# Optimization experiments

Measured on AMD Instinct MI355X. Metric: run time of the kernel, lower is better.

## Reference

```python
import jax, jax.numpy as jnp
import numpy as np

N, E, D, R = 50000, 600000, 128, 8


def rgcn_conv(x, src, dst, etype, W, root, bias):
    """PyG-style RGCNConv with mean aggregation per relation.
    x: [N, Din]; W: [R, Din, Dout]; root: [Din, Dout]; bias: [Dout]."""
    n = x.shape[0]
    r = W.shape[0]
    # Transform once per relation at node level (cheaper than per-edge matmul).
    xw = jnp.einsum('nd,rdo->rno', x, W)  # [R, N, Dout]
    # Per-(relation, target) edge counts for mean normalization.
    seg = etype * n + dst                  # combined segment id in [0, R*N)
    counts = jax.ops.segment_sum(jnp.ones(src.shape, dtype=x.dtype), seg,
                                 num_segments=r * n)
    norm = 1.0 / jnp.maximum(counts[seg], 1.0)   # [E]
    msg = xw[etype, src] * norm[:, None]          # gather per edge, [E, Dout]
    agg = jax.ops.segment_sum(msg, dst, num_segments=n)  # scatter-add, [N, Dout]
    return agg + x @ root + bias


def setup_inputs() -> dict:
    key = jax.random.key(0)
    ks = jax.random.split(key, 16)
    s = 1.0 / np.sqrt(D)
    inp = {
        'x': jax.random.normal(ks[0], (N, D), dtype=jnp.float32),
        'edge_index': jax.random.randint(ks[1], (2, E), 0, N, dtype=jnp.int32),
        'edge_type': jax.random.randint(ks[2], (E,), 0, R, dtype=jnp.int32),
        'W1': jax.random.normal(ks[3], (R, D, D), dtype=jnp.float32) * s,
        'root1': jax.random.normal(ks[4], (D, D), dtype=jnp.float32) * s,
        'b1': jnp.zeros((D,), dtype=jnp.float32),
        'W2': jax.random.normal(ks[5], (R, D, D), dtype=jnp.float32) * s,
        'root2': jax.random.normal(ks[6], (D, D), dtype=jnp.float32) * s,
        'b2': jnp.zeros((D,), dtype=jnp.float32),
        'W3': jax.random.normal(ks[7], (R, D, D), dtype=jnp.float32) * s,
        'root3': jax.random.normal(ks[8], (D, D), dtype=jnp.float32) * s,
        'b3': jnp.zeros((D,), dtype=jnp.float32),
        'res_w': jax.random.normal(ks[9], (D, D), dtype=jnp.float32) * s,
        'res_b': jnp.zeros((D,), dtype=jnp.float32),
    }
    return inp


def reference(x, edge_index, edge_type, W1, root1, b1, W2, root2, b2,
              W3, root3, b3, res_w, res_b):
    src, dst = edge_index[0], edge_index[1]
    res = x @ res_w + res_b
    h = jax.nn.relu(rgcn_conv(x, src, dst, edge_type, W1, root1, b1))
    h = res + jax.nn.relu(h)
    h = jax.nn.relu(rgcn_conv(h, src, dst, edge_type, W2, root2, b2))
    h = res + jax.nn.relu(h)
    h = jax.nn.relu(rgcn_conv(h, src, dst, edge_type, W3, root3, b3))
    h = res + jax.nn.relu(h)
    # Dropout(0.05) is identity in eval mode.
    return h
```

## Files before the change

### kernel.cpp

```cpp
#include <hip/hip_runtime.h>
#include <hip/hip_bf16.h>

#define NN 50000
#define EE 600000
#define RR 8
#define NSEG (NN*RR)
#define NB_SCAN ((NSEG + 1023)/1024)
#define RSTRIDE 2320

typedef unsigned int u32;
typedef __attribute__((ext_vector_type(8))) short bf16x8;
typedef __attribute__((ext_vector_type(4))) float f32x4;
typedef __attribute__((ext_vector_type(2))) float f32x2;
typedef __attribute__((ext_vector_type(4))) u32 u32x4;

__device__ inline unsigned short f2bf(float f){
  u32 u = __float_as_uint(f);
  u32 r = (u + 0x7fffu + ((u >> 16) & 1u)) >> 16;
  return (unsigned short)r;
}
__device__ inline float bf2f(unsigned short b){ return __uint_as_float((u32)b << 16); }

__global__ void cvt_k(const float* __restrict__ in, unsigned short* __restrict__ out, int n4){
  int i = blockIdx.x * 256 + threadIdx.x;
  if (i >= n4) return;
  float4 v = ((const float4*)in)[i];
  ushort4 o;
  o.x = f2bf(v.x); o.y = f2bf(v.y); o.z = f2bf(v.z); o.w = f2bf(v.w);
  ((ushort4*)out)[i] = o;
}

__global__ void packall_k(const float* __restrict__ W1, const float* __restrict__ r1,
                          const float* __restrict__ W2, const float* __restrict__ r2,
                          const float* __restrict__ W3, const float* __restrict__ r3,
                          const float* __restrict__ rw,
                          short* __restrict__ Bp1, short* __restrict__ Bp2,
                          short* __restrict__ Bp3, short* __restrict__ BpR){
  int tid = blockIdx.x * 256 + threadIdx.x;
  if (tid >= 112 * 512) return;
  int unit = tid >> 9;
  const float* Wrel; const float* root; short* Bp; int k32; int krel;
  if      (unit < 36){ Wrel = W1; root = r1; Bp = Bp1; k32 = unit;       krel = 1024; }
  else if (unit < 72){ Wrel = W2; root = r2; Bp = Bp2; k32 = unit - 36;  krel = 1024; }
  else if (unit <108){ Wrel = W3; root = r3; Bp = Bp3; k32 = unit - 72;  krel = 1024; }
  else               { Wrel = rw; root = rw; Bp = BpR; k32 = unit - 108; krel = 0;    }
  int lane = tid & 63;
  int nf   = (tid >> 6) & 7;
  int col  = nf * 16 + (lane & 15);
  short vals[8];
#pragma unroll
  for (int i = 0; i < 8; ++i){
    int kk = k32 * 32 + ((lane >> 4) << 3) + i;
    float f = (kk < krel) ? Wrel[(size_t)kk * 128 + col]
                          : root[(size_t)(kk - krel) * 128 + col];
    vals[i] = (short)f2bf(f);
  }
  *(bf16x8*)(Bp + (size_t)(k32 * 512 + (tid & 511)) * 8) = *(const bf16x8*)vals;
}

__global__ void count_k(const int* __restrict__ dst, const int* __restrict__ et,
                        u32* __restrict__ cnt){
  int e = blockIdx.x * 256 + threadIdx.x;
  if (e >= EE) return;
  atomicAdd(&cnt[(size_t)et[e] * NN + dst[e]], 1u);
}

__global__ void scan1_k(const u32* __restrict__ cnt, u32* __restrict__ offs, u32* __restrict__ bsum){
  __shared__ u32 s[512];
  int t = threadIdx.x;
  int base = blockIdx.x * 1024 + t * 4;
  u32 loc[4]; u32 sum = 0;
#pragma unroll
  for (int i = 0; i < 4; ++i){ loc[i] = (base + i < NSEG) ? cnt[base + i] : 0u; sum += loc[i]; }
  int pb = 0;
  s[t] = sum; __syncthreads();
  for (int off = 1; off < 256; off <<= 1){
    u32 v = s[pb * 256 + t];
    if (t >= off) v += s[pb * 256 + t - off];
    s[(pb ^ 1) * 256 + t] = v; pb ^= 1; __syncthreads();
  }
  u32 incl = s[pb * 256 + t];
  u32 excl = incl - sum;
  if (t == 255) bsum[blockIdx.x] = incl;
  u32 run = excl;
#pragma unroll
  for (int i = 0; i < 4; ++i){ if (base + i < NSEG) offs[base + i] = run; run += loc[i]; }
}

__global__ void scan2_k(u32* __restrict__ bsum){
  __shared__ u32 s[1024];
  int t = threadIdx.x;
  u32 v = (t < NB_SCAN) ? bsum[t] : 0u;
  int pb = 0;
  s[t] = v; __syncthreads();
  for (int off = 1; off < 512; off <<= 1){
    u32 x = s[pb * 512 + t];
    if (t >= off) x += s[pb * 512 + t - off];
    s[(pb ^ 1) * 512 + t] = x; pb ^= 1; __syncthreads();
  }
  u32 incl = s[pb * 512 + t];
  if (t < NB_SCAN) bsum[t] = incl - v;
}

__global__ void scan3_k(u32* __restrict__ offs, const u32* __restrict__ bsum){
  int t = threadIdx.x;
  int base = blockIdx.x * 1024 + t * 4;
  u32 add = bsum[blockIdx.x];
#pragma unroll
  for (int i = 0; i < 4; ++i){ if (base + i < NSEG) offs[base + i] += add; }
  if (blockIdx.x == 0 && t == 0) offs[NSEG] = EE;
}

__global__ void fill_k(const int* __restrict__ src, const int* __restrict__ dst,
                       const int* __restrict__ et, const u32* __restrict__ offs,
                       u32* __restrict__ cnt, int* __restrict__ elist){
  int e = blockIdx.x * 256 + threadIdx.x;
  if (e >= EE) return;
  int s = et[e] * NN + dst[e];
  u32 p = atomicSub(&cnt[s], 1u);
  elist[offs[s] + p - 1] = src[e];
}

__launch_bounds__(256, 4)
__global__ void resg_k(const unsigned short* __restrict__ xb, const short* __restrict__ Bp,
                       const float* __restrict__ rb, unsigned short* __restrict__ resb){
  const int tid = threadIdx.x;
  const int w = tid >> 6, l = tid & 63;
  const int sub = l >> 4, llr = l & 15;
  const int rowbase = blockIdx.x * 64 + w * 16;
  int vr = rowbase + llr; if (vr > NN - 1) vr = NN - 1;
  f32x4 acc[8] = {};
#pragma unroll
  for (int t = 0; t < 4; ++t){
    bf16x8 af = *(const bf16x8*)(xb + (size_t)vr * 128 + (t * 4 + sub) * 8);
    const short* bb = Bp + (size_t)(t * 8) * 512 + l * 8;
#pragma unroll
    for (int nf = 0; nf < 8; ++nf){
      bf16x8 bq = *(const bf16x8*)(bb + nf * 512);
      acc[nf] = __builtin_amdgcn_mfma_f32_16x16x32_bf16(af, bq, acc[nf], 0, 0, 0);
    }
  }
  const int lr = l >> 4, lc = l & 15;
#pragma unroll
  for (int nf = 0; nf < 8; ++nf){
    int col = nf * 16 + lc;
    float bv = rb[col];
#pragma unroll
    for (int r = 0; r < 4; ++r){
      int row = rowbase + lr * 4 + r;
      if (row < NN) resb[(size_t)row * 128 + col] = f2bf(acc[nf][r] + bv);
    }
  }
}

#define ACC1(P0, P1) do{ \
  _Pragma("unroll") \
  for (int i_ = 0; i_ < 4; ++i_){ \
    f32x2 a_, b_; \
    a_[0] = __uint_as_float((P0)[i_] << 16); \
    a_[1] = __uint_as_float((P0)[i_] & 0xffff0000u); \
    b_[0] = __uint_as_float((P1)[i_] << 16); \
    b_[1] = __uint_as_float((P1)[i_] & 0xffff0000u); \
    s0[i_] += a_; s1[i_] += b_; \
  } }while(0)

__device__ __forceinline__ void gather_seg(u32 beg, u32 end,
                                           const unsigned short* __restrict__ hb,
                                           const int* __restrict__ elist,
                                           char* __restrict__ Ab,
                                           int row, int rseg, int ll8){
  f32x2 s0[4], s1[4];
#pragma unroll
  for (int i = 0; i < 4; ++i){ s0[i] = (f32x2){0.f,0.f}; s1[i] = (f32x2){0.f,0.f}; }
  u32 e = beg;
  for (; e + 4 <= end; e += 4){
    int q0 = elist[e], q1 = elist[e+1], q2 = elist[e+2], q3 = elist[e+3];
    const unsigned short* r0 = hb + (size_t)q0 * 128;
    const unsigned short* r1 = hb + (size_t)q1 * 128;
    const unsigned short* r2 = hb + (size_t)q2 * 128;
    const unsigned short* r3 = hb + (size_t)q3 * 128;
    u32x4 p00 = *(const u32x4*)r0, p01 = *(const u32x4*)(r0 + 8);
    u32x4 p10 = *(const u32x4*)r1, p11 = *(const u32x4*)(r1 + 8);
    u32x4 p20 = *(const u32x4*)r2, p21 = *(const u32x4*)(r2 + 8);
    u32x4 p30 = *(const u32x4*)r3, p31 = *(const u32x4*)(r3 + 8);
    ACC1(p00, p01); ACC1(p10, p11); ACC1(p20, p21); ACC1(p30, p31);
  }
  if (e + 2 <= end){
    int q0 = elist[e], q1 = elist[e+1];
    const unsigned short* r0 = hb + (size_t)q0 * 128;
    const unsigned short* r1 = hb + (size_t)q1 * 128;
    u32x4 p00 = *(const u32x4*)r0, p01 = *(const u32x4*)(r0 + 8);
    u32x4 p10 = *(const u32x4*)r1, p11 = *(const u32x4*)(r1 + 8);
    ACC1(p00, p01); ACC1(p10, p11);
    e += 2;
  }
  if (e < end){
    int q0 = elist[e];
    const unsigned short* r0 = hb + (size_t)q0 * 128;
    u32x4 p00 = *(const u32x4*)r0, p01 = *(const u32x4*)(r0 + 8);
    ACC1(p00, p01);
  }
  u32 deg = end - beg;
  if (deg){
    float inv = __builtin_amdgcn_rcpf((float)deg);
#pragma unroll
    for (int i = 0; i < 4; ++i){ s0[i] *= inv; s1[i] *= inv; }
  }
  u32x4 o0, o1;
#pragma unroll
  for (int i = 0; i < 4; ++i){
    o0[i] = (u32)f2bf(s0[i][0]) | ((u32)f2bf(s0[i][1]) << 16);
    o1[i] = (u32)f2bf(s1[i][0]) | ((u32)f2bf(s1[i][1]) << 16);
  }
  char* wp = Ab + row * RSTRIDE + (rseg * 16 + ll8 * 2) * 16;
  *(u32x4*)wp = o0;
  *(u32x4*)(wp + 16) = o1;
}

template<int OUTMODE>
__launch_bounds__(1024, 8)
__global__ void fused_k(const u32* __restrict__ offs, const int* __restrict__ elist,
                        const unsigned short* __restrict__ h,
                        const short* __restrict__ Bp,
                        const float* __restrict__ bias,
                        const unsigned short* __restrict__ resb,
                        float* __restrict__ outf, unsigned short* __restrict__ outb){
  __shared__ char Ab[32 * RSTRIDE];
  const int tid = threadIdx.x;
  const int mbase = blockIdx.x * 32;

  {
    const int g = tid >> 3, ll8 = tid & 7;
    const unsigned short* hb = h + (size_t)ll8 * 16;
    int r0 = g >> 5, row0 = g & 31;
    int t1 = g + 128;
    int r1 = t1 >> 5, row1 = t1 & 31;
    int v0 = mbase + row0; if (v0 > NN - 1) v0 = NN - 1;
    int v1 = mbase + row1; if (v1 > NN - 1) v1 = NN - 1;
    size_t sg0 = (size_t)r0 * NN + v0, sg1 = (size_t)r1 * NN + v1;
    u32 b0 = offs[sg0], e0 = offs[sg0 + 1];
    u32 b1 = offs[sg1], e1 = offs[sg1 + 1];
    gather_seg(b0, e0, hb, elist, Ab, row0, r0, ll8);
    gather_seg(b1, e1, hb, elist, Ab, row1, r1, ll8);
    if (g < 32){
      int row = g;
      int v = mbase + row; if (v > NN - 1) v = NN - 1;
      const unsigned short* rp = h + (size_t)v * 128 + ll8 * 16;
      u32x4 o0 = *(const u32x4*)rp, o1 = *(const u32x4*)(rp + 8);
      char* wp = Ab + row * RSTRIDE + (128 + ll8 * 2) * 16;
      *(u32x4*)wp = o0;
      *(u32x4*)(wp + 16) = o1;
    }
  }
  __syncthreads();

  const int w = tid >> 6, l = tid & 63;
  if (w >= 8) return;
  const int mf = w >> 2, nq = w & 3;
  const int nf0 = nq * 2, nf1 = nq * 2 + 1;
  const int sub = l >> 4, llr = l & 15;
  const int rowb = mf * 16 + llr;
  f32x4 acc0 = {}, acc1 = {};
#pragma unroll 6
  for (int kt = 0; kt < 18; ++kt){
#pragma unroll
    for (int t = 0; t < 2; ++t){
      int ks = kt * 8 + t * 4 + sub;
      bf16x8 af = *(const bf16x8*)(Ab + rowb * RSTRIDE + ks * 16);
      const short* bb = Bp + ((size_t)((kt * 2 + t) * 8)) * 512 + l * 8;
      bf16x8 bq0 = *(const bf16x8*)(bb + nf0 * 512);
      bf16x8 bq1 = *(const bf16x8*)(bb + nf1 * 512);
      acc0 = __builtin_amdgcn_mfma_f32_16x16x32_bf16(af, bq0, acc0, 0, 0, 0);
      acc1 = __builtin_amdgcn_mfma_f32_16x16x32_bf16(af, bq1, acc1, 0, 0, 0);
    }
  }

  const int lr = l >> 4, lc = l & 15;
#pragma unroll
  for (int half = 0; half < 2; ++half){
    int col = (half ? nf1 : nf0) * 16 + lc;
    float bv = bias[col];
    const f32x4& ac = half ? acc1 : acc0;
#pragma unroll
    for (int r = 0; r < 4; ++r){
      int row = mbase + mf * 16 + lr * 4 + r;
      if (row < NN){
        float v = ac[r] + bv;
        v = bf2f(resb[(size_t)row * 128 + col]) + fmaxf(v, 0.f);
        if (OUTMODE == 1) outb[(size_t)row * 128 + col] = f2bf(v);
        else              outf[(size_t)row * 128 + col] = v;
      }
    }
  }
}

extern "C" void kernel_launch(void* const* d_in, const int* in_sizes, int n_in,
                              void* d_out, int out_size, void* d_ws, size_t ws_size,
                              hipStream_t stream){
  const float* x  = (const float*)d_in[0];
  const int*   ei = (const int*)d_in[1];
  const int*   et = (const int*)d_in[2];
  const float* W1 = (const float*)d_in[3];
  const float* r1 = (const float*)d_in[4];
  const float* b1 = (const float*)d_in[5];
  const float* W2 = (const float*)d_in[6];
  const float* r2 = (const float*)d_in[7];
  const float* b2 = (const float*)d_in[8];
  const float* W3 = (const float*)d_in[9];
  const float* r3 = (const float*)d_in[10];
  const float* b3 = (const float*)d_in[11];
  const float* rw = (const float*)d_in[12];
  const float* rb = (const float*)d_in[13];
  const int* srcv = ei;
  const int* dstv = ei + EE;

  char* p = (char*)d_ws;
  auto take = [&](size_t b)->char*{ char* q = p; p += (b + 255) & ~(size_t)255; return q; };
  unsigned short* xb   = (unsigned short*)take((size_t)NN * 128 * 2);
  unsigned short* h1   = (unsigned short*)take((size_t)NN * 128 * 2);
  unsigned short* h2   = (unsigned short*)take((size_t)NN * 128 * 2);
  unsigned short* resb = (unsigned short*)take((size_t)NN * 128 * 2);
  short* Bp1 = (short*)take(36 * 4096 * 2);
  short* Bp2 = (short*)take(36 * 4096 * 2);
  short* Bp3 = (short*)take(36 * 4096 * 2);
  short* BpR = (short*)take(4 * 4096 * 2);
  u32* cnt   = (u32*)take((size_t)NSEG * 4);
  u32* offs  = (u32*)take((size_t)(NSEG + 1) * 4);
  int* elist = (int*)take((size_t)EE * 4);
  u32* bsum  = (u32*)take((size_t)NB_SCAN * 4);

  hipMemsetAsync(cnt, 0, (size_t)NSEG * 4, stream);

  cvt_k<<<(NN * 128 / 4 + 255) / 256, 256, 0, stream>>>(x, xb, NN * 128 / 4);
  packall_k<<<(112 * 512 + 255) / 256, 256, 0, stream>>>(W1, r1, W2, r2, W3, r3, rw,
                                                         Bp1, Bp2, Bp3, BpR);

  count_k<<<(EE + 255) / 256, 256, 0, stream>>>(dstv, et, cnt);
  scan1_k<<<NB_SCAN, 256, 0, stream>>>(cnt, offs, bsum);
  scan2_k<<<1, 512, 0, stream>>>(bsum);
  scan3_k<<<NB_SCAN, 256, 0, stream>>>(offs, bsum);
  fill_k<<<(EE + 255) / 256, 256, 0, stream>>>(srcv, dstv, et, offs, cnt, elist);

  const int GB = (NN + 31) / 32;

  resg_k<<<(NN + 63) / 64, 256, 0, stream>>>(xb, BpR, rb, resb);

  fused_k<1><<<GB, 1024, 0, stream>>>(offs, elist, xb, Bp1, b1, resb, nullptr, h1);
  fused_k<1><<<GB, 1024, 0, stream>>>(offs, elist, h1, Bp2, b2, resb, nullptr, h2);
  fused_k<2><<<GB, 1024, 0, stream>>>(offs, elist, h2, Bp3, b3, resb, (float*)d_out, nullptr);
}
```

Before: 308.8 us.

## Shrink fused RGCN tile to 16 rows with 512-thread blocks

Changes the fused gather+GEMM kernel from 32-row tiles with 1024 threads to 16-row tiles with 512 threads. In the old layout half the waves exited after the gather; now all 8 waves do MFMA work, each on one 16-column fragment. LDS per block is halved and the grid doubles, which should give more blocks per CU and better latency hiding for the irregular gather. The cost is that each B fragment is reloaded by twice as many blocks, and the tail bounds checks are dropped because N is divisible by 16.

Measured after the change: 285.1 us. -7.7%, faster.

```diff
diff --git a/kernel.cpp b/kernel.cpp
--- a/kernel.cpp
+++ b/kernel.cpp
@@ -218,36 +218,32 @@
 }
 
 template<int OUTMODE>
-__launch_bounds__(1024, 8)
+__launch_bounds__(512, 4)
 __global__ void fused_k(const u32* __restrict__ offs, const int* __restrict__ elist,
                         const unsigned short* __restrict__ h,
                         const short* __restrict__ Bp,
                         const float* __restrict__ bias,
                         const unsigned short* __restrict__ resb,
                         float* __restrict__ outf, unsigned short* __restrict__ outb){
-  __shared__ char Ab[32 * RSTRIDE];
+  __shared__ char Ab[16 * RSTRIDE];
   const int tid = threadIdx.x;
-  const int mbase = blockIdx.x * 32;
+  const int mbase = blockIdx.x * 16;
 
   {
     const int g = tid >> 3, ll8 = tid & 7;
     const unsigned short* hb = h + (size_t)ll8 * 16;
-    int r0 = g >> 5, row0 = g & 31;
-    int t1 = g + 128;
-    int r1 = t1 >> 5, row1 = t1 & 31;
-    int v0 = mbase + row0; if (v0 > NN - 1) v0 = NN - 1;
-    int v1 = mbase + row1; if (v1 > NN - 1) v1 = NN - 1;
-    size_t sg0 = (size_t)r0 * NN + v0, sg1 = (size_t)r1 * NN + v1;
+    int r0 = g >> 4, row = g & 15;
+    int r1 = r0 + 4;
+    int v = mbase + row;
+    size_t sg0 = (size_t)r0 * NN + v, sg1 = (size_t)r1 * NN + v;
     u32 b0 = offs[sg0], e0 = offs[sg0 + 1];
     u32 b1 = offs[sg1], e1 = offs[sg1 + 1];
-    gather_seg(b0, e0, hb, elist, Ab, row0, r0, ll8);
-    gather_seg(b1, e1, hb, elist, Ab, row1, r1, ll8);
-    if (g < 32){
-      int row = g;
-      int v = mbase + row; if (v > NN - 1) v = NN - 1;
-      const unsigned short* rp = h + (size_t)v * 128 + ll8 * 16;
+    gather_seg(b0, e0, hb, elist, Ab, row, r0, ll8);
+    gather_seg(b1, e1, hb, elist, Ab, row, r1, ll8);
+    if (g < 16){
+      const unsigned short* rp = h + (size_t)(mbase + g) * 128 + ll8 * 16;
       u32x4 o0 = *(const u32x4*)rp, o1 = *(const u32x4*)(rp + 8);
-      char* wp = Ab + row * RSTRIDE + (128 + ll8 * 2) * 16;
+      char* wp = Ab + g * RSTRIDE + (128 + ll8 * 2) * 16;
       *(u32x4*)wp = o0;
       *(u32x4*)(wp + 16) = o1;
     }
@@ -255,42 +251,30 @@
   __syncthreads();
 
   const int w = tid >> 6, l = tid & 63;
-  if (w >= 8) return;
-  const int mf = w >> 2, nq = w & 3;
-  const int nf0 = nq * 2, nf1 = nq * 2 + 1;
+  const int nf = w;
   const int sub = l >> 4, llr = l & 15;
-  const int rowb = mf * 16 + llr;
-  f32x4 acc0 = {}, acc1 = {};
+  f32x4 acc = {};
 #pragma unroll 6
   for (int kt = 0; kt < 18; ++kt){
 #pragma unroll
     for (int t = 0; t < 2; ++t){
       int ks = kt * 8 + t * 4 + sub;
-      bf16x8 af = *(const bf16x8*)(Ab + rowb * RSTRIDE + ks * 16);
-      const short* bb = Bp + ((size_t)((kt * 2 + t) * 8)) * 512 + l * 8;
-      bf16x8 bq0 = *(const bf16x8*)(bb + nf0 * 512);
-      bf16x8 bq1 = *(const bf16x8*)(bb + nf1 * 512);
-      acc0 = __builtin_amdgcn_mfma_f32_16x16x32_bf16(af, bq0, acc0, 0, 0, 0);
-      acc1 = __builtin_amdgcn_mfma_f32_16x16x32_bf16(af, bq1, acc1, 0, 0, 0);
+      bf16x8 af = *(const bf16x8*)(Ab + llr * RSTRIDE + ks * 16);
+      bf16x8 bq = *(const bf16x8*)(Bp + ((size_t)((kt * 2 + t) * 8 + nf)) * 512 + l * 8);
+      acc = __builtin_amdgcn_mfma_f32_16x16x32_bf16(af, bq, acc, 0, 0, 0);
     }
   }
 
   const int lr = l >> 4, lc = l & 15;
-#pragma unroll
-  for (int half = 0; half < 2; ++half){
-    int col = (half ? nf1 : nf0) * 16 + lc;
-    float bv = bias[col];
-    const f32x4& ac = half ? acc1 : acc0;
-#pragma unroll
-    for (int r = 0; r < 4; ++r){
-      int row = mbase + mf * 16 + lr * 4 + r;
-      if (row < NN){
-        float v = ac[r] + bv;
-        v = bf2f(resb[(size_t)row * 128 + col]) + fmaxf(v, 0.f);
-        if (OUTMODE == 1) outb[(size_t)row * 128 + col] = f2bf(v);
-        else              outf[(size_t)row * 128 + col] = v;
-      }
-    }
+  int col = nf * 16 + lc;
+  float bv = bias[col];
+#pragma unroll
+  for (int r = 0; r < 4; ++r){
+    int row = mbase + lr * 4 + r;
+    float v = acc[r] + bv;
+    v = bf2f(resb[(size_t)row * 128 + col]) + fmaxf(v, 0.f);
+    if (OUTMODE == 1) outb[(size_t)row * 128 + col] = f2bf(v);
+    else              outf[(size_t)row * 128 + col] = v;
   }
 }
 
@@ -341,11 +325,11 @@
   scan3_k<<<NB_SCAN, 256, 0, stream>>>(offs, bsum);
   fill_k<<<(EE + 255) / 256, 256, 0, stream>>>(srcv, dstv, et, offs, cnt, elist);
 
-  const int GB = (NN + 31) / 32;
+  const int GB = NN / 16;
 
   resg_k<<<(NN + 63) / 64, 256, 0, stream>>>(xb, BpR, rb, resb);
 
-  fused_k<1><<<GB, 1024, 0, stream>>>(offs, elist, xb, Bp1, b1, resb, nullptr, h1);
-  fused_k<1><<<GB, 1024, 0, stream>>>(offs, elist, h1, Bp2, b2, resb, nullptr, h2);
-  fused_k<2><<<GB, 1024, 0, stream>>>(offs, elist, h2, Bp3, b3, resb, (float*)d_out, nullptr);
-}
+  fused_k<1><<<GB, 512, 0, stream>>>(offs, elist, xb, Bp1, b1, resb, nullptr, h1);
+  fused_k<1><<<GB, 512, 0, stream>>>(offs, elist, h1, Bp2, b2, resb, nullptr, h2);
+  fused_k<2><<<GB, 512, 0, stream>>>(offs, elist, h2, Bp3, b3, resb, (float*)d_out, nullptr);
+}
```
